# Performance work log

Measured on AMD Instinct MI355X. Metric: run time of the kernel, lower is better.

## Reference

```python
import jax, jax.numpy as jnp
import numpy as np

N = 50_000          # num nodes
E = 800_000         # num edges
D = 32              # input/hidden dim
NUM_LAYERS = 6
BOUNDARY_FILL = 100.0


def setup_inputs() -> dict:
    key = jax.random.key(0)
    ks = jax.random.split(key, 10)
    return {
        "node_in": jax.random.randint(ks[0], (E,), 0, N, dtype=jnp.int32),
        "node_out": jax.random.randint(ks[1], (E,), 0, N, dtype=jnp.int32),
        "edge_weight": jax.random.uniform(ks[2], (E,), dtype=jnp.float32),
        "h_index": 0,
        "query_weight": jax.random.normal(ks[3], (1, D), dtype=jnp.float32) * 0.1,
        "rel_W": jax.random.normal(ks[4], (NUM_LAYERS, D, D), dtype=jnp.float32) / np.sqrt(D),
        "rel_b": jnp.zeros((NUM_LAYERS, D), dtype=jnp.float32),
        "lin_W": jax.random.normal(ks[5], (NUM_LAYERS, 13 * D, D), dtype=jnp.float32) / np.sqrt(13 * D),
        "lin_b": jnp.zeros((NUM_LAYERS, D), dtype=jnp.float32),
        "mlp_W1": jax.random.normal(ks[6], (2 * D, 2 * D), dtype=jnp.float32) / np.sqrt(2 * D),
        "mlp_b1": jnp.zeros((2 * D,), dtype=jnp.float32),
        "mlp_W2": jax.random.normal(ks[7], (2 * D, 1), dtype=jnp.float32) / np.sqrt(2 * D),
        "mlp_b2": jnp.zeros((1,), dtype=jnp.float32),
    }


def reference(node_in, node_out, edge_weight, h_index, query_weight,
              rel_W, rel_b, lin_W, lin_b, mlp_W1, mlp_b1, mlp_W2, mlp_b2):
    # query = self.query(r_index) with r_index = 0, batch = 1
    query = query_weight[:1]                                # [1, D]
    boundary = jnp.full((N, 1, D), BOUNDARY_FILL, dtype=jnp.float32)
    boundary = boundary.at[h_index, 0].set(0.0)             # boundary[h][0] = 0

    loop = jnp.arange(N, dtype=node_out.dtype)
    node_in_aug = jnp.concatenate([node_in, loop])          # boundary rows act as self-loop msgs
    node_out_aug = jnp.concatenate([node_out, loop])
    ew_aug = jnp.concatenate([edge_weight, jnp.ones((N,), edge_weight.dtype)])

    degree_out = jax.ops.segment_sum(edge_weight, node_out, num_segments=N) + 1.0  # [N]
    count = jax.ops.segment_sum(jnp.ones_like(ew_aug), node_out_aug, num_segments=N)  # [N]

    # PNA degree scalers (identity / amplification / attenuation)
    scale = jnp.log(degree_out)
    scale = scale / jnp.mean(scale)
    scales = jnp.stack([jnp.ones_like(scale), scale, 1.0 / jnp.clip(scale, 1e-2)], axis=-1)  # [N,3]

    w = ew_aug[:, None, None]
    cnt = count[:, None, None]

    layer_input = boundary
    predecessor = jnp.zeros((N,), dtype=node_in.dtype)
    for i in range(NUM_LAYERS):
        # dependent relation embedding: relation_linear(query), relation id 0 everywhere
        rel_input = query @ rel_W[i] + rel_b[i]             # [1, D]
        message = layer_input[node_in] * rel_input[None]    # [E,1,D] distmult
        msg_aug = jnp.concatenate([message, boundary], axis=0)  # [E+N,1,D]
        wm = msg_aug * w

        mean = jax.ops.segment_sum(wm, node_out_aug, num_segments=N) / cnt
        sq_mean = jax.ops.segment_sum(jnp.square(msg_aug) * w, node_out_aug, num_segments=N) / cnt
        mx = jax.ops.segment_max(wm, node_out_aug, num_segments=N)
        mn = jax.ops.segment_min(wm, node_out_aug, num_segments=N)
        std = jnp.sqrt(jnp.clip(sq_mean - jnp.square(mean), 1e-6))

        feats = jnp.stack([mean, mx, mn, std], axis=-1).reshape(N, 1, 4 * D)
        update = (feats[..., None] * scales[:, None, None, :]).reshape(N, 1, 12 * D)
        hidden = jax.nn.relu(
            jnp.concatenate([layer_input, update], axis=-1) @ lin_W[i] + lin_b[i]
        )  # [N,1,D]

        if i == NUM_LAYERS - 1:
            # predecessor: source node of the strongest incoming (weighted) message
            msg_score = wm.sum(axis=(1, 2))                 # [E+N]
            seg_max = jax.ops.segment_max(msg_score, node_out_aug, num_segments=N)
            cand = jnp.where(msg_score >= seg_max[node_out_aug], node_in_aug,
                             jnp.asarray(N, node_in_aug.dtype))
            predecessor = jax.ops.segment_min(cand, node_out_aug, num_segments=N)
        layer_input = hidden

    node_query = jnp.broadcast_to(query[None], (N, 1, D))
    output = jnp.concatenate([layer_input, node_query], axis=-1)  # [N,1,2D]
    feature = jnp.transpose(output, (1, 0, 2))                    # [1,N,2D]
    h = jax.nn.relu(feature @ mlp_W1 + mlp_b1)
    score = (h @ mlp_W2 + mlp_b2).squeeze(-1)                     # [1,N]
    return score, predecessor
```

## Files before the change

### kernel.cpp

```cpp
#include <hip/hip_runtime.h>
#include <math.h>

#define NN 50000
#define EE 800000
#define DD 32
#define BSTR 64
#define NPART 8
#define CPB 128

typedef float v2f __attribute__((ext_vector_type(2)));


__global__ __launch_bounds__(256) void k_zero(float* p, int count){
  int i = blockIdx.x*256 + threadIdx.x;
  if (i < count) p[i] = 0.f;
}

__global__ __launch_bounds__(256) void k_fillcsr(const int* __restrict__ node_in,
                                                 const int* __restrict__ node_out,
                                                 const float* __restrict__ ew,
                                                 int* __restrict__ cursor,
                                                 int2* __restrict__ csr){
  int part  = blockIdx.x & (NPART-1);
  int group = blockIdx.x >> 3;
  const int per = (EE + CPB - 1) / CPB;
  int e0 = group * per;
  int e1 = (e0 + per < EE) ? (e0 + per) : EE;
  unsigned lo = (unsigned)part * 6250u;
  unsigned hi = lo + 6250u;
  for (int e = e0 + threadIdx.x; e < e1; e += 256){
    unsigned o = (unsigned)node_out[e];
    if (o >= lo && o < hi){
      int pos = atomicAdd(&cursor[o], 1);
      int2 v; v.x = node_in[e]; v.y = __float_as_int(ew[e]);
      csr[o*BSTR + pos] = v;
    }
  }
}

__global__ __launch_bounds__(256) void k_sumw(int2* __restrict__ csr,
                                              const int* __restrict__ cursor,
                                              float* __restrict__ deg_w,
                                              float* __restrict__ logsum){
  __shared__ float sf[256];
  int t = threadIdx.x;
  int g = t >> 3, lane = t & 7;
  int n = blockIdx.x*32 + g;
  float s = 0.f;
  if (n < NN){
    int deg = cursor[n];
    int2* row = csr + n*BSTR;
    for (int i = lane; i < deg; i += 8) s += __int_as_float(row[i].y);
    s += __shfl_xor(s, 1);
    s += __shfl_xor(s, 2);
    s += __shfl_xor(s, 4);
    row[deg + lane] = make_int2(0, 0);
    if (lane == 0) deg_w[n] = s;
  }
  sf[t] = (n < NN && lane == 0) ? logf(s + 1.f) : 0.f;
  __syncthreads();
  for (int off = 128; off > 0; off >>= 1){
    if (t < off) sf[t] += sf[t+off];
    __syncthreads();
  }
  if (t == 0) atomicAdd(logsum, sf[0]);
}

__global__ __launch_bounds__(320) void k_prep(const float* __restrict__ qw,
                                              const float* __restrict__ rel_W,
                                              const float* __restrict__ rel_b,
                                              const float* __restrict__ W1,
                                              const float* __restrict__ b1,
                                              const float* __restrict__ lin_W,
                                              float* __restrict__ rel6,
                                              float* __restrict__ qc,
                                              float* __restrict__ wcol){
  int t = threadIdx.x;
  if (t < 192){
    int l = t >> 5, j = t & 31;
    float s = rel_b[t];
    for (int d = 0; d < 32; ++d) s += qw[d] * rel_W[l*1024 + d*32 + j];
    rel6[t] = s;
  } else if (t < 256){
    int j = t - 192;
    float s = b1[j];
    for (int k = 0; k < 32; ++k) s += qw[k] * W1[(32+k)*64 + j];
    qc[j] = s;
  } else if (t < 288){
    int j = t - 256;
    float s = 0.f;
    for (int k = 0; k < 32; ++k) s += lin_W[k*32 + j];
    wcol[j] = s;
  }
}

__global__ __launch_bounds__(256) void k_dot(const float* __restrict__ h,
                                             const float* __restrict__ rel6,
                                             float* __restrict__ tdot){
  int n0 = blockIdx.x*256 + threadIdx.x;
  int n = (n0 < NN) ? n0 : NN-1;
  const float* relr = rel6 + 5*32;
  float s = 0.f;
  #pragma unroll
  for (int d = 0; d < 32; ++d) s += h[n*32 + d] * relr[d];
  if (n0 < NN) tdot[n0] = s;
}

__global__ __launch_bounds__(512, 6) void k_layer0(const float* __restrict__ rel6,
                                               const int* __restrict__ cursor,
                                               const int2* __restrict__ csr,
                                               const int* __restrict__ hidx,
                                               const float* __restrict__ lin_W,
                                               const float* __restrict__ lin_b,
                                               const float* __restrict__ wcol,
                                               const float* __restrict__ deg_w,
                                               const float* __restrict__ logsum,
                                               float* __restrict__ h_next){
  __shared__ float sh[128*65];
  int tid = threadIdx.x;
  int base = blockIdx.x * 64;
  int hv0 = *hidx;

  {
    int nl   = tid >> 3;
    int quad = tid & 7;
    float4 r4 = ((const float4*)(rel6))[quad];
    int n0 = base + nl;
    int n = (n0 < NN) ? n0 : NN-1;
    int deg = cursor[n];
    int s0 = n*BSTR, s1 = s0 + deg;
    float S1=0.f, S2=0.f, M=-INFINITY, m=INFINITY;

#define ACCS(C) { \
    float w  = __int_as_float(C.y); \
    float hv = (C.x == hv0) ? 0.f : 100.f; \
    float wm = w * hv; \
    S1 += wm; S2 += wm * hv; \
    M = fmaxf(M, wm); m = fminf(m, wm); }

    int2 cA = csr[s0],   cB = csr[s0+1], cC = csr[s0+2], cD = csr[s0+3];
    int e = s0;
    for (; e + 4 <= s1; e += 4){
      int2 nA = csr[e+4], nB = csr[e+5], nC = csr[e+6], nD = csr[e+7];
      ACCS(cA) ACCS(cB) ACCS(cC) ACCS(cD)
      cA = nA; cB = nB; cC = nC; cD = nD;
    }
    if (e < s1){
      ACCS(cA)
      if (e + 1 < s1){
        ACCS(cB)
        if (e + 2 < s1) ACCS(cC)
      }
    }
#undef ACCS

    float bnd = (n == hv0) ? 0.f : 100.f;
    float cntf = (float)(deg + 1);
#define FIN(cc, rc) { \
    float mxv, mnv; \
    if (deg > 0){ \
      float em = (rc >= 0.f) ? rc*M : rc*m; \
      float en = (rc >= 0.f) ? rc*m : rc*M; \
      mxv = fmaxf(em, bnd); mnv = fminf(en, bnd); \
    } else { mxv = bnd; mnv = bnd; } \
    float meanv = (rc*S1 + bnd) / cntf; \
    float sq    = (rc*rc*S2 + bnd*bnd) / cntf; \
    float sdv   = sqrtf(fmaxf(sq - meanv*meanv, 1e-6f)); \
    int d = quad*4 + cc; \
    sh[(d*4+0)*65 + nl] = meanv; \
    sh[(d*4+1)*65 + nl] = mxv; \
    sh[(d*4+2)*65 + nl] = mnv; \
    sh[(d*4+3)*65 + nl] = sdv; }
    FIN(0, r4.x) FIN(1, r4.y) FIN(2, r4.z) FIN(3, r4.w)
#undef FIN
  }
  __syncthreads();

  {
    const float* Wl = lin_W;
    int lane = tid & 63;
    int j0 = __builtin_amdgcn_readfirstlane((tid >> 6) * 4);
    int n0 = base + lane;
    int n = (n0 < NN) ? n0 : NN-1;
    float mean = *logsum / (float)NN;
    float sc = logf(deg_w[n] + 1.f) / mean;
    float iv = 1.f / fmaxf(sc, 0.01f);
    float bndn = (n == hv0) ? 0.f : 100.f;
    v2f a01p={0,0}, a23p={0,0}, a01s={0,0}, a23s={0,0}, a01i={0,0}, a23i={0,0};

    for (int kp = 0; kp < 128; ++kp){
      float f = sh[kp*65 + lane];
      int d = kp >> 2, c = kp & 3;
      const v2f* w2 = (const v2f*)(Wl + (32 + d*12 + c*3)*32 + j0);
      v2f fv; fv[0]=f; fv[1]=f;
      a01p += fv*w2[0];  a23p += fv*w2[1];
      a01s += fv*w2[16]; a23s += fv*w2[17];
      a01i += fv*w2[32]; a23i += fv*w2[33];
    }
    v2f sc2; sc2[0]=sc; sc2[1]=sc;
    v2f iv2; iv2[0]=iv; iv2[1]=iv;
    v2f a01 = a01p + sc2*a01s + iv2*a01i;
    v2f a23 = a23p + sc2*a23s + iv2*a23i;
    a01[0] += lin_b[j0+0] + bndn*wcol[j0+0];
    a01[1] += lin_b[j0+1] + bndn*wcol[j0+1];
    a23[0] += lin_b[j0+2] + bndn*wcol[j0+2];
    a23[1] += lin_b[j0+3] + bndn*wcol[j0+3];

    if (n0 < NN){
      float vs[4] = { a01[0], a01[1], a23[0], a23[1] };
      #pragma unroll
      for (int j = 0; j < 4; ++j)
        h_next[n0*32 + j0 + j] = fmaxf(vs[j], 0.f);
    }
  }
}

template<bool PRED>
__global__ __launch_bounds__(512, 6) void k_layer(const float* __restrict__ h,
                                               const float* __restrict__ rel6,
                                               const int* __restrict__ cursor,
                                               const int2* __restrict__ csr,
                                               const int* __restrict__ hidx,
                                               const float* __restrict__ tdot,
                                               const float* __restrict__ lin_W,
                                               const float* __restrict__ lin_b,
                                               const float* __restrict__ deg_w,
                                               const float* __restrict__ logsum,
                                               float* __restrict__ h_next,
                                               float* __restrict__ pred_out,
                                               const float* __restrict__ qc,
                                               const float* __restrict__ W1,
                                               const float* __restrict__ W2,
                                               const float* __restrict__ b2,
                                               float* __restrict__ out_score,
                                               int l){
  __shared__ float sh[128*65];
  int tid = threadIdx.x;
  int base = blockIdx.x * 64;
  int hv0 = *hidx;

  {
    int nl   = tid >> 3;
    int quad = tid & 7;
    float4 r4 = ((const float4*)(rel6 + l*32))[quad];
    int n0 = base + nl;
    bool valid = n0 < NN;
    int n = valid ? n0 : NN-1;
    int deg = cursor[n];
    int s0 = n*BSTR, s1 = s0 + deg;
    v2f S1xy={0,0}, S1zw={0,0}, S2xy={0,0}, S2zw={0,0};
    float M0=-INFINITY,M1=-INFINITY,M2=-INFINITY,M3=-INFINITY;
    float m0=INFINITY,m1=INFINITY,m2=INFINITY,m3=INFINITY;
    float best=-INFINITY; int bi=NN;

#define ACC1(C, A, T) { \
    float w = __int_as_float(C.y); \
    v2f wv; wv[0]=w; wv[1]=w; \
    v2f axy; axy[0]=A.x; axy[1]=A.y; \
    v2f azw; azw[0]=A.z; azw[1]=A.w; \
    v2f pxy = wv*axy, pzw = wv*azw; \
    S1xy += pxy; S1zw += pzw; \
    S2xy += pxy*axy; S2zw += pzw*azw; \
    M0=fmaxf(M0,pxy[0]); M1=fmaxf(M1,pxy[1]); M2=fmaxf(M2,pzw[0]); M3=fmaxf(M3,pzw[1]); \
    m0=fminf(m0,pxy[0]); m1=fminf(m1,pxy[1]); m2=fminf(m2,pzw[0]); m3=fminf(m3,pzw[1]); \
    if (PRED){ \
      float sv = w*T; \
      if (sv > best){ best = sv; bi = C.x; } \
      else if (sv == best && C.x < bi) bi = C.x; \
    } }

    int2 cA = csr[s0],   cB = csr[s0+1], cC = csr[s0+2], cD = csr[s0+3];
    int e = s0;
    for (; e + 4 <= s1; e += 4){
      float4 a  = ((const float4*)(h + cA.x*32))[quad];
      float4 b  = ((const float4*)(h + cB.x*32))[quad];
      float4 c4 = ((const float4*)(h + cC.x*32))[quad];
      float4 d4 = ((const float4*)(h + cD.x*32))[quad];
      float tA=0.f, tB=0.f, tC=0.f, tD=0.f;
      if (PRED){ tA = tdot[cA.x]; tB = tdot[cB.x]; tC = tdot[cC.x]; tD = tdot[cD.x]; }
      int2 nA = csr[e+4], nB = csr[e+5], nC = csr[e+6], nD = csr[e+7];
      ACC1(cA, a, tA)
      ACC1(cB, b, tB)
      ACC1(cC, c4, tC)
      ACC1(cD, d4, tD)
      cA = nA; cB = nB; cC = nC; cD = nD;
    }
    if (e < s1){
      float4 a = ((const float4*)(h + cA.x*32))[quad];
      float tA = 0.f; if (PRED) tA = tdot[cA.x];
      ACC1(cA, a, tA)
      if (e + 1 < s1){
        float4 b = ((const float4*)(h + cB.x*32))[quad];
        float tB = 0.f; if (PRED) tB = tdot[cB.x];
        ACC1(cB, b, tB)
        if (e + 2 < s1){
          float4 c4 = ((const float4*)(h + cC.x*32))[quad];
          float tC = 0.f; if (PRED) tC = tdot[cC.x];
          ACC1(cC, c4, tC)
        }
      }
    }
#undef ACC1

    float bnd = (n == hv0) ? 0.f : 100.f;
    float cntf = (float)(deg + 1);
#define FIN(cc, rc, S1c, S2c, Mc, mc) { \
    float mxv, mnv; \
    if (deg > 0){ \
      float em = (rc >= 0.f) ? rc*Mc : rc*mc; \
      float en = (rc >= 0.f) ? rc*mc : rc*Mc; \
      mxv = fmaxf(em, bnd); mnv = fminf(en, bnd); \
    } else { mxv = bnd; mnv = bnd; } \
    float meanv = (rc*S1c + bnd) / cntf; \
    float sq    = (rc*rc*S2c + bnd*bnd) / cntf; \
    float sdv   = sqrtf(fmaxf(sq - meanv*meanv, 1e-6f)); \
    int d = quad*4 + cc; \
    sh[(d*4+0)*65 + nl] = meanv; \
    sh[(d*4+1)*65 + nl] = mxv; \
    sh[(d*4+2)*65 + nl] = mnv; \
    sh[(d*4+3)*65 + nl] = sdv; }
    FIN(0, r4.x, S1xy[0], S2xy[0], M0, m0)
    FIN(1, r4.y, S1xy[1], S2xy[1], M1, m1)
    FIN(2, r4.z, S1zw[0], S2zw[0], M2, m2)
    FIN(3, r4.w, S1zw[1], S2zw[1], M3, m3)
#undef FIN
    if (PRED && valid && quad == 0){
      float ss = (n == hv0) ? 0.f : 3200.f;
      if (ss > best){ best = ss; bi = n; }
      else if (ss == best && n < bi) bi = n;
      pred_out[n] = (float)bi;
    }
  }
  __syncthreads();

  {
    const float* Wl = lin_W + (size_t)l * 13312;
    int lane = tid & 63;
    int j0 = __builtin_amdgcn_readfirstlane((tid >> 6) * 4);
    int n0 = base + lane;
    int n = (n0 < NN) ? n0 : NN-1;
    float mean = *logsum / (float)NN;
    float sc = logf(deg_w[n] + 1.f) / mean;
    float iv = 1.f / fmaxf(sc, 0.01f);
    const float4* hr = (const float4*)(h + (size_t)n*32);
    float4 x0=hr[0],x1=hr[1],x2=hr[2],x3=hr[3],x4=hr[4],x5=hr[5],x6=hr[6],x7=hr[7];
    v2f a01p={0,0}, a23p={0,0}, a01s={0,0}, a23s={0,0}, a01i={0,0}, a23i={0,0};

#define KONE(XV, K) { \
    v2f xv2; xv2[0] = XV; xv2[1] = XV; \
    const v2f* wr2 = (const v2f*)(Wl + (K)*32 + j0); \
    a01p += xv2 * wr2[0]; \
    a23p += xv2 * wr2[1]; }
#define KQ(X, KB) KONE(X.x, KB+0) KONE(X.y, KB+1) KONE(X.z, KB+2) KONE(X.w, KB+3)
    KQ(x0, 0) KQ(x1, 4) KQ(x2, 8) KQ(x3, 12)
    KQ(x4, 16) KQ(x5, 20) KQ(x6, 24) KQ(x7, 28)
#undef KQ
#undef KONE

    for (int kp = 0; kp < 128; ++kp){
      float f = sh[kp*65 + lane];
      int d = kp >> 2, c = kp & 3;
      const v2f* w2 = (const v2f*)(Wl + (32 + d*12 + c*3)*32 + j0);
      v2f fv; fv[0]=f; fv[1]=f;
      a01p += fv*w2[0];  a23p += fv*w2[1];
      a01s += fv*w2[16]; a23s += fv*w2[17];
      a01i += fv*w2[32]; a23i += fv*w2[33];
    }
    v2f sc2; sc2[0]=sc; sc2[1]=sc;
    v2f iv2; iv2[0]=iv; iv2[1]=iv;
    v2f a01 = a01p + sc2*a01s + iv2*a01i;
    v2f a23 = a23p + sc2*a23s + iv2*a23i;
    a01[0] += lin_b[l*32 + j0 + 0];
    a01[1] += lin_b[l*32 + j0 + 1];
    a23[0] += lin_b[l*32 + j0 + 2];
    a23[1] += lin_b[l*32 + j0 + 3];

    float v0r = fmaxf(a01[0], 0.f), v1r = fmaxf(a01[1], 0.f);
    float v2r = fmaxf(a23[0], 0.f), v3r = fmaxf(a23[1], 0.f);

    if (!PRED){
      if (n0 < NN){
        h_next[n0*32 + j0 + 0] = v0r;
        h_next[n0*32 + j0 + 1] = v1r;
        h_next[n0*32 + j0 + 2] = v2r;
        h_next[n0*32 + j0 + 3] = v3r;
      }
    } else {
      __syncthreads();
      sh[(j0+0)*65 + lane] = v0r;
      sh[(j0+1)*65 + lane] = v1r;
      sh[(j0+2)*65 + lane] = v2r;
      sh[(j0+3)*65 + lane] = v3r;
      __syncthreads();
      int node = tid & 63;
      int grp  = __builtin_amdgcn_readfirstlane(tid >> 6);
      int jm = grp*8;
      v2f b0, b1v, b2v, b3;
      b0[0]=qc[jm+0]; b0[1]=qc[jm+1]; b1v[0]=qc[jm+2]; b1v[1]=qc[jm+3];
      b2v[0]=qc[jm+4]; b2v[1]=qc[jm+5]; b3[0]=qc[jm+6]; b3[1]=qc[jm+7];
      for (int k = 0; k < 32; ++k){
        float xv = sh[k*65 + node];
        const v2f* wr = (const v2f*)(W1 + k*64 + jm);
        v2f xv2; xv2[0]=xv; xv2[1]=xv;
        b0 += xv2*wr[0]; b1v += xv2*wr[1]; b2v += xv2*wr[2]; b3 += xv2*wr[3];
      }
      float part = fmaxf(b0[0],0.f)*W2[jm+0] + fmaxf(b0[1],0.f)*W2[jm+1]
                 + fmaxf(b1v[0],0.f)*W2[jm+2] + fmaxf(b1v[1],0.f)*W2[jm+3]
                 + fmaxf(b2v[0],0.f)*W2[jm+4] + fmaxf(b2v[1],0.f)*W2[jm+5]
                 + fmaxf(b3[0],0.f)*W2[jm+6] + fmaxf(b3[1],0.f)*W2[jm+7];
      sh[2080 + node*9 + grp] = part;
      __syncthreads();
      if (tid < 64){
        float s = b2[0];
        #pragma unroll
        for (int g = 0; g < 8; ++g) s += sh[2080 + tid*9 + g];
        if (base + tid < NN) out_score[base + tid] = s;
      }
    }
  }
}

extern "C" void kernel_launch(void* const* d_in, const int* in_sizes, int n_in,
                              void* d_out, int out_size, void* d_ws, size_t ws_size,
                              hipStream_t stream){
  const int*   node_in  = (const int*)d_in[0];
  const int*   node_out = (const int*)d_in[1];
  const float* ew       = (const float*)d_in[2];
  const int*   hidx     = (const int*)d_in[3];
  const float* qw       = (const float*)d_in[4];
  const float* rel_W    = (const float*)d_in[5];
  const float* rel_b    = (const float*)d_in[6];
  const float* lin_W    = (const float*)d_in[7];
  const float* lin_b    = (const float*)d_in[8];
  const float* W1       = (const float*)d_in[9];
  const float* b1       = (const float*)d_in[10];
  const float* W2       = (const float*)d_in[11];
  const float* b2       = (const float*)d_in[12];
  float* out_score = (float*)d_out;
  float* out_pred  = out_score + NN;

  char* w = (char*)d_ws;
  size_t off = 0;
  auto take = [&](size_t bytes)->char*{
    char* p = w + off;
    off = (off + bytes + 255) & ~(size_t)255;
    return p;
  };
  size_t bucket_elems = (size_t)NN * BSTR;
  int2*  csr      = (int2*)take(bucket_elems*8);
  char*  zb       = take((size_t)NN*4 + (size_t)NN*4 + 256);
  int*   cursor   = (int*)zb;
  float* deg_w    = (float*)(cursor + NN);
  float* logsum   = (float*)(deg_w + NN);
  int zc = NN + NN + 64;

  float* rel6      = (float*)take(192*4);
  float* qc        = (float*)take(64*4);
  float* wcol      = (float*)take(32*4);
  float* tdot      = (float*)take((size_t)NN*4);
  float* h_a       = (float*)take((size_t)NN*32*4);
  float* h_b       = (float*)take((size_t)NN*32*4);

  int nb  = (NN + 255) / 256;
  int nsb = (NN + 31) / 32;
  int nlb = (NN + 63) / 64;
  k_zero   <<<(zc+255)/256, 256, 0, stream>>>((float*)zb, zc);
  k_fillcsr<<<NPART*CPB, 256, 0, stream>>>(node_in, node_out, ew, cursor, csr);
  k_sumw   <<<nsb, 256, 0, stream>>>(csr, cursor, deg_w, logsum);
  k_prep   <<<1, 320, 0, stream>>>(qw, rel_W, rel_b, W1, b1, lin_W, rel6, qc, wcol);

  k_layer0<<<nlb, 512, 0, stream>>>(rel6, cursor, csr, hidx, lin_W, lin_b,
                                    wcol, deg_w, logsum, h_a);

  float* hc = h_a;
  float* hn = h_b;
  for (int l = 1; l < 6; ++l){
    if (l == 5){
      k_dot<<<nb, 256, 0, stream>>>(hc, rel6, tdot);
      k_layer<true><<<nlb, 512, 0, stream>>>(hc, rel6, cursor, csr, hidx, tdot,
                                             lin_W, lin_b, deg_w, logsum,
                                             hn, out_pred,
                                             qc, W1, W2, b2, out_score, l);
    } else {
      k_layer<false><<<nlb, 512, 0, stream>>>(hc, rel6, cursor, csr, hidx, tdot,
                                              lin_W, lin_b, deg_w, logsum,
                                              hn, out_pred,
                                              qc, W1, W2, b2, out_score, l);
    }
    float* t1 = hc; hc = hn; hn = t1;
  }
}
```

Measured before the change: 425.8 us.

## Software-pipeline neighbor gathers and store stats row-major as float4 in LDS

```diff
diff --git a/kernel.cpp b/kernel.cpp
--- a/kernel.cpp
+++ b/kernel.cpp
@@ -106,6 +106,8 @@
   if (n0 < NN) tdot[n0] = s;
 }
 
+#define SROW 132
+
 __global__ __launch_bounds__(512, 6) void k_layer0(const float* __restrict__ rel6,
                                                const int* __restrict__ cursor,
                                                const int2* __restrict__ csr,
@@ -116,7 +118,7 @@
                                                const float* __restrict__ deg_w,
                                                const float* __restrict__ logsum,
                                                float* __restrict__ h_next){
-  __shared__ float sh[128*65];
+  __shared__ __align__(16) float sh[64*SROW];
   int tid = threadIdx.x;
   int base = blockIdx.x * 64;
   int hv0 = *hidx;
@@ -167,10 +169,8 @@
     float sq    = (rc*rc*S2 + bnd*bnd) / cntf; \
     float sdv   = sqrtf(fmaxf(sq - meanv*meanv, 1e-6f)); \
     int d = quad*4 + cc; \
-    sh[(d*4+0)*65 + nl] = meanv; \
-    sh[(d*4+1)*65 + nl] = mxv; \
-    sh[(d*4+2)*65 + nl] = mnv; \
-    sh[(d*4+3)*65 + nl] = sdv; }
+    float4 o; o.x = meanv; o.y = mxv; o.z = mnv; o.w = sdv; \
+    *(float4*)(sh + nl*SROW + d*4) = o; }
     FIN(0, r4.x) FIN(1, r4.y) FIN(2, r4.z) FIN(3, r4.w)
 #undef FIN
   }
@@ -188,14 +188,20 @@
     float bndn = (n == hv0) ? 0.f : 100.f;
     v2f a01p={0,0}, a23p={0,0}, a01s={0,0}, a23s={0,0}, a01i={0,0}, a23i={0,0};
 
-    for (int kp = 0; kp < 128; ++kp){
-      float f = sh[kp*65 + lane];
-      int d = kp >> 2, c = kp & 3;
-      const v2f* w2 = (const v2f*)(Wl + (32 + d*12 + c*3)*32 + j0);
-      v2f fv; fv[0]=f; fv[1]=f;
-      a01p += fv*w2[0];  a23p += fv*w2[1];
-      a01s += fv*w2[16]; a23s += fv*w2[17];
-      a01i += fv*w2[32]; a23i += fv*w2[33];
+#define CSTAT(dd, cc, fv) { \
+    const v2f* w2 = (const v2f*)(Wl + (32 + (dd)*12 + (cc)*3)*32 + j0); \
+    v2f fvv; fvv[0]=(fv); fvv[1]=(fv); \
+    a01p += fvv*w2[0];  a23p += fvv*w2[1]; \
+    a01s += fvv*w2[16]; a23s += fvv*w2[17]; \
+    a01i += fvv*w2[32]; a23i += fvv*w2[33]; }
+
+    const float4* frow = (const float4*)(sh + lane*SROW);
+    for (int d = 0; d < 32; d += 4){
+      float4 fa = frow[d], fb = frow[d+1], fc = frow[d+2], fd = frow[d+3];
+      CSTAT(d+0,0,fa.x) CSTAT(d+0,1,fa.y) CSTAT(d+0,2,fa.z) CSTAT(d+0,3,fa.w)
+      CSTAT(d+1,0,fb.x) CSTAT(d+1,1,fb.y) CSTAT(d+1,2,fb.z) CSTAT(d+1,3,fb.w)
+      CSTAT(d+2,0,fc.x) CSTAT(d+2,1,fc.y) CSTAT(d+2,2,fc.z) CSTAT(d+2,3,fc.w)
+      CSTAT(d+3,0,fd.x) CSTAT(d+3,1,fd.y) CSTAT(d+3,2,fd.z) CSTAT(d+3,3,fd.w)
     }
     v2f sc2; sc2[0]=sc; sc2[1]=sc;
     v2f iv2; iv2[0]=iv; iv2[1]=iv;
@@ -234,7 +240,7 @@
                                                const float* __restrict__ b2,
                                                float* __restrict__ out_score,
                                                int l){
-  __shared__ float sh[128*65];
+  __shared__ __align__(16) float sh[64*SROW];
   int tid = threadIdx.x;
   int base = blockIdx.x * 64;
   int hv0 = *hidx;
@@ -253,6 +259,7 @@
     float m0=INFINITY,m1=INFINITY,m2=INFINITY,m3=INFINITY;
     float best=-INFINITY; int bi=NN;
 
+#define GATH(C) (((const float4*)(h + (size_t)(C).x*32))[quad])
 #define ACC1(C, A, T) { \
     float w = __int_as_float(C.y); \
     v2f wv; wv[0]=w; wv[1]=w; \
@@ -269,38 +276,51 @@
       else if (sv == best && C.x < bi) bi = C.x; \
     } }
 
-    int2 cA = csr[s0],   cB = csr[s0+1], cC = csr[s0+2], cD = csr[s0+3];
+    int2 cA = csr[s0], cB = csr[s0+1], cC = csr[s0+2], cD = csr[s0+3];
+    float4 gA = GATH(cA), gB = GATH(cB), gC = GATH(cC), gD = GATH(cD);
+    float tA=0.f, tB=0.f, tC=0.f, tD=0.f;
+    if (PRED){ tA = tdot[cA.x]; tB = tdot[cB.x]; tC = tdot[cC.x]; tD = tdot[cD.x]; }
     int e = s0;
-    for (; e + 4 <= s1; e += 4){
-      float4 a  = ((const float4*)(h + cA.x*32))[quad];
-      float4 b  = ((const float4*)(h + cB.x*32))[quad];
-      float4 c4 = ((const float4*)(h + cC.x*32))[quad];
-      float4 d4 = ((const float4*)(h + cD.x*32))[quad];
-      float tA=0.f, tB=0.f, tC=0.f, tD=0.f;
-      if (PRED){ tA = tdot[cA.x]; tB = tdot[cB.x]; tC = tdot[cC.x]; tD = tdot[cD.x]; }
+    for (; e + 8 <= s1; e += 4){
       int2 nA = csr[e+4], nB = csr[e+5], nC = csr[e+6], nD = csr[e+7];
-      ACC1(cA, a, tA)
-      ACC1(cB, b, tB)
-      ACC1(cC, c4, tC)
-      ACC1(cD, d4, tD)
+      float4 hA = GATH(nA), hB = GATH(nB), hC = GATH(nC), hD = GATH(nD);
+      float uA=0.f, uB=0.f, uC=0.f, uD=0.f;
+      if (PRED){ uA = tdot[nA.x]; uB = tdot[nB.x]; uC = tdot[nC.x]; uD = tdot[nD.x]; }
+      ACC1(cA, gA, tA)
+      ACC1(cB, gB, tB)
+      ACC1(cC, gC, tC)
+      ACC1(cD, gD, tD)
       cA = nA; cB = nB; cC = nC; cD = nD;
-    }
-    if (e < s1){
-      float4 a = ((const float4*)(h + cA.x*32))[quad];
-      float tA = 0.f; if (PRED) tA = tdot[cA.x];
-      ACC1(cA, a, tA)
-      if (e + 1 < s1){
-        float4 b = ((const float4*)(h + cB.x*32))[quad];
-        float tB = 0.f; if (PRED) tB = tdot[cB.x];
-        ACC1(cB, b, tB)
-        if (e + 2 < s1){
-          float4 c4 = ((const float4*)(h + cC.x*32))[quad];
-          float tC = 0.f; if (PRED) tC = tdot[cC.x];
-          ACC1(cC, c4, tC)
+      gA = hA; gB = hB; gC = hC; gD = hD;
+      tA = uA; tB = uB; tC = uC; tD = uD;
+    }
+    int rem = s1 - e;
+    if (rem > 0){
+      ACC1(cA, gA, tA)
+      if (rem > 1) ACC1(cB, gB, tB)
+      if (rem > 2) ACC1(cC, gC, tC)
+      if (rem > 3) ACC1(cD, gD, tD)
+      if (rem > 4){
+        int2 pA = csr[e+4];
+        float4 qA = GATH(pA);
+        float vA = 0.f; if (PRED) vA = tdot[pA.x];
+        ACC1(pA, qA, vA)
+        if (rem > 5){
+          int2 pB = csr[e+5];
+          float4 qB = GATH(pB);
+          float vB = 0.f; if (PRED) vB = tdot[pB.x];
+          ACC1(pB, qB, vB)
+          if (rem > 6){
+            int2 pC = csr[e+6];
+            float4 qC = GATH(pC);
+            float vC = 0.f; if (PRED) vC = tdot[pC.x];
+            ACC1(pC, qC, vC)
+          }
         }
       }
     }
 #undef ACC1
+#undef GATH
 
     float bnd = (n == hv0) ? 0.f : 100.f;
     float cntf = (float)(deg + 1);
@@ -315,10 +335,8 @@
     float sq    = (rc*rc*S2c + bnd*bnd) / cntf; \
     float sdv   = sqrtf(fmaxf(sq - meanv*meanv, 1e-6f)); \
     int d = quad*4 + cc; \
-    sh[(d*4+0)*65 + nl] = meanv; \
-    sh[(d*4+1)*65 + nl] = mxv; \
-    sh[(d*4+2)*65 + nl] = mnv; \
-    sh[(d*4+3)*65 + nl] = sdv; }
+    float4 o; o.x = meanv; o.y = mxv; o.z = mnv; o.w = sdv; \
+    *(float4*)(sh + nl*SROW + d*4) = o; }
     FIN(0, r4.x, S1xy[0], S2xy[0], M0, m0)
     FIN(1, r4.y, S1xy[1], S2xy[1], M1, m1)
     FIN(2, r4.z, S1zw[0], S2zw[0], M2, m2)
@@ -357,14 +375,13 @@
 #undef KQ
 #undef KONE
 
-    for (int kp = 0; kp < 128; ++kp){
-      float f = sh[kp*65 + lane];
-      int d = kp >> 2, c = kp & 3;
-      const v2f* w2 = (const v2f*)(Wl + (32 + d*12 + c*3)*32 + j0);
-      v2f fv; fv[0]=f; fv[1]=f;
-      a01p += fv*w2[0];  a23p += fv*w2[1];
-      a01s += fv*w2[16]; a23s += fv*w2[17];
-      a01i += fv*w2[32]; a23i += fv*w2[33];
+    const float4* frow = (const float4*)(sh + lane*SROW);
+    for (int d = 0; d < 32; d += 4){
+      float4 fa = frow[d], fb = frow[d+1], fc = frow[d+2], fd = frow[d+3];
+      CSTAT(d+0,0,fa.x) CSTAT(d+0,1,fa.y) CSTAT(d+0,2,fa.z) CSTAT(d+0,3,fa.w)
+      CSTAT(d+1,0,fb.x) CSTAT(d+1,1,fb.y) CSTAT(d+1,2,fb.z) CSTAT(d+1,3,fb.w)
+      CSTAT(d+2,0,fc.x) CSTAT(d+2,1,fc.y) CSTAT(d+2,2,fc.z) CSTAT(d+2,3,fc.w)
+      CSTAT(d+3,0,fd.x) CSTAT(d+3,1,fd.y) CSTAT(d+3,2,fd.z) CSTAT(d+3,3,fd.w)
     }
     v2f sc2; sc2[0]=sc; sc2[1]=sc;
     v2f iv2; iv2[0]=iv; iv2[1]=iv;
```

New measurement: 533.6 us. 25.3% more time.
